# Kernel optimization log

Measured on AMD Instinct MI355X. Metric: run time of the kernel, lower is better.

The kernel has to match this reference:

```python
import jax, jax.numpy as jnp
import numpy as np

E, K = 8, 2            # num_experts, top-k
I, H, O = 1024, 4096, 1024  # input_dim, hidden_dim, output_dim
N = 8192               # batch (tokens)


def _ln(x, g, b, eps=1e-5):
    # torch nn.LayerNorm: biased variance
    m = x.mean(-1, keepdims=True)
    v = x.var(-1, keepdims=True)
    return (x - m) * jax.lax.rsqrt(v + eps) * g + b


def setup_inputs() -> dict:
    key = jax.random.key(0)
    ks = jax.random.split(key, 8)
    s = lambda i, shape, scale: jax.random.normal(ks[i], shape, jnp.float32) * scale
    return dict(
        x=s(0, (N, I), 1.0),
        w1=s(1, (E, I, H), I ** -0.5),
        b1=jnp.zeros((E, H), jnp.float32),
        ln1_g=jnp.ones((E, H), jnp.float32),
        ln1_b=jnp.zeros((E, H), jnp.float32),
        w2=s(2, (E, H, O), H ** -0.5),
        b2=jnp.zeros((E, O), jnp.float32),
        wg=s(3, (I, E), I ** -0.5),
        bg=jnp.zeros((E,), jnp.float32),
        out_g=jnp.ones((O,), jnp.float32),
        out_b=jnp.zeros((O,), jnp.float32),
    )


def reference(x, w1, b1, ln1_g, ln1_b, w2, b2, wg, bg, out_g, out_b):
    n = x.shape[0]
    # gating: softmax -> top-k -> renormalize
    probs = jax.nn.softmax(x @ wg + bg, axis=-1)          # [N, E]
    topw, topi = jax.lax.top_k(probs, K)                  # [N, K]
    topw = topw / topw.sum(-1, keepdims=True)
    rows = jnp.arange(n)[:, None]
    combine = jnp.zeros((n, E), x.dtype).at[rows, topi].add(topw)  # [N, E]
    mask = jnp.zeros((n, E), x.dtype).at[rows, topi].set(1.0)      # [N, E]

    # expert dispatch + weighted combine; combine==0 for unrouted tokens,
    # mathematically identical to the torch gather/index_add loop (eval mode, dropout off)
    def step(acc, p):
        W1, B1, G, Bt, W2, B2, c = p
        h = jax.nn.gelu(_ln(x @ W1 + B1, G, Bt), approximate=False)  # [N, H]
        return acc + c[:, None] * (h @ W2 + B2), None

    out0 = jnp.zeros((n, w2.shape[-1]), x.dtype)
    out, _ = jax.lax.scan(step, out0, (w1, b1, ln1_g, ln1_b, w2, b2, combine.T))

    # aux load-balancing loss (torch .std() is unbiased, ddof=1)
    imp = probs.sum(0)
    imp_loss = (jnp.std(imp, ddof=1) / (imp.mean() + 1e-6)) ** 2
    load = mask.mean(0)
    load_loss = (jnp.std(load, ddof=1) / (load.mean() + 1e-6)) ** 2
    aux = imp_loss + load_loss

    out = _ln(out, out_g, out_b)
    return out, aux
```

## Files before the change

### kernel.cpp

```cpp
#include <hip/hip_runtime.h>

#define NTOK 8192
#define IDIM 1024
#define HDIM 4096
#define ODIM 1024
#define NEXP 8
#define ROWCAP 18432
#define MBLK 72
#define GATE_BLOCKS 512

typedef unsigned short u16;
typedef __attribute__((ext_vector_type(8))) __bf16 bf16x8;
typedef __attribute__((ext_vector_type(8))) short short8;
typedef __attribute__((ext_vector_type(4))) float f32x4;
typedef __attribute__((ext_vector_type(4))) unsigned short u16x4;
typedef __attribute__((ext_vector_type(8))) unsigned short u16x8;

__device__ __forceinline__ u16 f2bf(float f) {
  union { float f; unsigned u; } c; c.f = f;
  unsigned u = c.u;
  return (u16)((u + 0x7fffu + ((u >> 16) & 1u)) >> 16);
}
__device__ __forceinline__ float bf2f(u16 h) {
  union { unsigned u; float f; } c; c.u = ((unsigned)h) << 16;
  return c.f;
}
__device__ __forceinline__ void gload16(const void* g, void* l) {
  __builtin_amdgcn_global_load_lds((const __attribute__((address_space(1))) unsigned*)g,
                                   (__attribute__((address_space(3))) unsigned*)l, 16, 0, 0);
}

#define BARR __builtin_amdgcn_s_barrier()
#define LGKM0 asm volatile("s_waitcnt lgkmcnt(0)" ::: "memory")
#define VMW4 asm volatile("s_waitcnt vmcnt(4)" ::: "memory")
#define VMW0 asm volatile("s_waitcnt vmcnt(0)" ::: "memory")
#define CFENCE asm volatile("" ::: "memory")

#define QUAD(AF, BF, MB, NBQ)                                                   \
  _Pragma("unroll") for (int kk = 0; kk < 2; ++kk)                              \
  _Pragma("unroll") for (int f = 0; f < 4; ++f)                                 \
  _Pragma("unroll") for (int n = 0; n < 2; ++n)                                 \
    acc[(MB) + f][(NBQ) + n] = __builtin_amdgcn_mfma_f32_16x16x32_bf16(         \
        AF[f][kk], BF[n][kk], acc[(MB) + f][(NBQ) + n], 0, 0, 0);

__global__ __launch_bounds__(256) void transpose_convert_kernel(
    const float* __restrict__ w1, const float* __restrict__ w2,
    u16* __restrict__ w1t, u16* __restrict__ w2t) {
  __shared__ __align__(16) unsigned char ldsb[32768];
  int bid = blockIdx.x;
  const float* in; u16* outp; int R, C, r0, c0;
  if (bid < 2048) {
    int e = bid >> 8, t = bid & 255;
    in = w1 + (size_t)e * IDIM * HDIM; outp = w1t + (size_t)e * IDIM * HDIM;
    R = IDIM; C = HDIM;
    r0 = (t >> 5) * 128; c0 = (t & 31) * 128;
  } else {
    int b2 = bid - 2048;
    int e = b2 >> 8, t = b2 & 255;
    in = w2 + (size_t)e * HDIM * ODIM; outp = w2t + (size_t)e * HDIM * ODIM;
    R = HDIM; C = ODIM;
    r0 = (t >> 3) * 128; c0 = (t & 7) * 128;
  }
  int tid = threadIdx.x;
  int rr = tid >> 5, cc = (tid & 31) * 4;
  #pragma unroll
  for (int it = 0; it < 16; ++it) {
    int r = it * 8 + rr;
    f32x4 v = *(const f32x4*)(in + (size_t)(r0 + r) * C + c0 + cc);
    u16x4 o;
    #pragma unroll
    for (int j = 0; j < 4; ++j) o[j] = f2bf(v[j]);
    unsigned a = ((unsigned)(r * 256 + cc * 2)) ^ ((((unsigned)r >> 3) & 7u) << 4);
    *(u16x4*)(ldsb + a) = o;
  }
  __syncthreads();
  int rc = tid & 15, cg = tid >> 4;
  #pragma unroll
  for (int i = 0; i < 8; ++i) {
    int c = cg + i * 16;
    u16x8 o;
    #pragma unroll
    for (int k = 0; k < 8; ++k) {
      int r = rc * 8 + k;
      unsigned a = ((unsigned)(r * 256 + c * 2)) ^ ((((unsigned)r >> 3) & 7u) << 4);
      o[k] = *(const u16*)(ldsb + a);
    }
    *(u16x8*)(outp + (size_t)(c0 + c) * R + r0 + rc * 8) = o;
  }
}

__global__ __launch_bounds__(256) void gating_kernel(
    const float* __restrict__ x, const float* __restrict__ wg, const float* __restrict__ bg,
    float* __restrict__ combine, float* __restrict__ imp_partial,
    int* __restrict__ sel, u16* __restrict__ xb) {
  __shared__ float wgs2[NEXP * IDIM];
  __shared__ float impw[4][NEXP];
  int tid = threadIdx.x;
  for (int d = tid; d < IDIM * NEXP; d += 256) {
    int i4 = d & 255, j = (d >> 8) & 3, e = d >> 10;
    wgs2[d] = wg[(i4 * 4 + j) * 8 + e];
  }
  __syncthreads();
  int wave = tid >> 6, lane = tid & 63;
  float impacc[NEXP];
  #pragma unroll
  for (int e = 0; e < NEXP; ++e) impacc[e] = 0.f;

  for (int it = 0; it < 4; ++it) {
    int t = blockIdx.x * 16 + wave * 4 + it;
    const float* xr = x + (size_t)t * IDIM;
    u16* xbw = xb + (size_t)t * IDIM;
    float s[NEXP];
    #pragma unroll
    for (int e = 0; e < NEXP; ++e) s[e] = 0.f;
    #pragma unroll
    for (int ii = 0; ii < 4; ++ii) {
      int base = ii * 256 + lane * 4;
      f32x4 xv = *(const f32x4*)(xr + base);
      u16x4 o;
      #pragma unroll
      for (int j = 0; j < 4; ++j) o[j] = f2bf(xv[j]);
      *(u16x4*)(xbw + base) = o;
      #pragma unroll
      for (int j = 0; j < 4; ++j) {
        int idx = j * 256 + ii * 64 + lane;
        #pragma unroll
        for (int e = 0; e < NEXP; ++e)
          s[e] = fmaf(xv[j], wgs2[e * 1024 + idx], s[e]);
      }
    }
    #pragma unroll
    for (int e = 0; e < NEXP; ++e) {
      #pragma unroll
      for (int off = 32; off; off >>= 1) s[e] += __shfl_xor(s[e], off);
    }
    if (lane == 0) {
      #pragma unroll
      for (int e = 0; e < NEXP; ++e) s[e] += bg[e];
      int i1 = 0; float v1 = s[0];
      #pragma unroll
      for (int e = 1; e < NEXP; ++e) if (s[e] > v1) { v1 = s[e]; i1 = e; }
      int i2 = -1; float v2 = -1e30f;
      #pragma unroll
      for (int e = 0; e < NEXP; ++e) if (e != i1 && s[e] > v2) { v2 = s[e]; i2 = e; }
      float p[NEXP], sum = 0.f;
      #pragma unroll
      for (int e = 0; e < NEXP; ++e) { p[e] = expf(s[e] - v1); sum += p[e]; }
      float inv = 1.f / sum;
      #pragma unroll
      for (int e = 0; e < NEXP; ++e) { p[e] *= inv; impacc[e] += p[e]; }
      float c1 = 1.f / (1.f + expf(v2 - v1));
      float c2 = 1.f - c1;
      #pragma unroll
      for (int e = 0; e < NEXP; ++e) combine[(size_t)t * NEXP + e] = 0.f;
      combine[(size_t)t * NEXP + i1] = c1;
      combine[(size_t)t * NEXP + i2] = c2;
      sel[t] = i1 | (i2 << 4);
    }
  }
  if (lane == 0) {
    #pragma unroll
    for (int e = 0; e < NEXP; ++e) impw[wave][e] = impacc[e];
  }
  __syncthreads();
  if (tid == 0) {
    #pragma unroll
    for (int e = 0; e < NEXP; ++e)
      imp_partial[blockIdx.x * NEXP + e] = impw[0][e] + impw[1][e] + impw[2][e] + impw[3][e];
  }
}

__global__ __launch_bounds__(256) void compact_kernel(
    const int* __restrict__ sel, int* __restrict__ tokenlist,
    int* __restrict__ cnt, int* __restrict__ pos) {
  __shared__ int warpsum[4];
  int e = blockIdx.x;
  int tid = threadIdx.x, lane = tid & 63, wave = tid >> 6;
  int base = 0;
  for (int chunk = 0; chunk < NTOK; chunk += 256) {
    int t = chunk + tid;
    int s = sel[t];
    int i1 = s & 15, i2 = s >> 4;
    bool m2 = (i2 == e);
    bool m = (i1 == e) || m2;
    unsigned long long bal = __ballot(m);
    int rank = __popcll(bal & ((1ull << lane) - 1ull));
    if (lane == 0) warpsum[wave] = __popcll(bal);
    __syncthreads();
    int woff = 0;
    #pragma unroll
    for (int w = 0; w < 4; ++w) if (w < wave) woff += warpsum[w];
    int total = warpsum[0] + warpsum[1] + warpsum[2] + warpsum[3];
    if (m) {
      int slot = base + woff + rank;
      tokenlist[e * NTOK + slot] = t;
      pos[t * 2 + (m2 ? 1 : 0)] = (e << 16) | slot;
    }
    base += total;
    __syncthreads();
  }
  if (tid == 0) cnt[e] = base;
}

__global__ __launch_bounds__(64) void offsets_aux_kernel(
    const int* __restrict__ cnt, const float* __restrict__ imp_partial,
    int* __restrict__ offsets, float* __restrict__ aux_out) {
  __shared__ float imp[NEXP];
  int tid = threadIdx.x;
  if (tid < NEXP) {
    float v = 0.f;
    for (int b = 0; b < GATE_BLOCKS; ++b) v += imp_partial[b * NEXP + tid];
    imp[tid] = v;
  }
  __syncthreads();
  if (tid == 0) {
    int off = 0;
    for (int e = 0; e < NEXP; ++e) { offsets[e] = off; off += (cnt[e] + 255) & ~255; }
    offsets[NEXP] = off;
    double im = 0.0;
    for (int e = 0; e < NEXP; ++e) im += imp[e];
    im /= NEXP;
    double iv = 0.0;
    for (int e = 0; e < NEXP; ++e) { double d = (double)imp[e] - im; iv += d * d; }
    iv /= (NEXP - 1);
    double il = sqrt(iv) / (im + 1e-6); il = il * il;
    double lm = 0.0;
    for (int e = 0; e < NEXP; ++e) lm += cnt[e];
    lm /= (double)NEXP * NTOK;
    double lv = 0.0;
    for (int e = 0; e < NEXP; ++e) { double d = (double)cnt[e] / NTOK - lm; lv += d * d; }
    lv /= (NEXP - 1);
    double ll = sqrt(lv) / (lm + 1e-6); ll = ll * ll;
    aux_out[0] = (float)(il + ll);
  }
}

__global__ __launch_bounds__(512, 2) void gemm1_kernel(
    const u16* __restrict__ xb, const u16* __restrict__ w1t, const float* __restrict__ b1,
    const int* __restrict__ tokenlist, const int* __restrict__ cnt,
    const int* __restrict__ offsets, u16* __restrict__ Hbuf) {
  __shared__ __align__(64) unsigned char sm[139264];
  const int NB = HDIM / 256;
  const int TT = IDIM / 64;
  int nwg = NB * MBLK;
  int flat = blockIdx.y * NB + blockIdx.x;
  int q = nwg >> 3;
  int swzb = (flat & 7) * q + (flat >> 3);
  int mb = swzb / NB, cb = swzb % NB;
  int grb = mb * 256;
  if (grb >= offsets[NEXP]) return;
  int e = 0;
  #pragma unroll
  for (int k = 0; k < NEXP - 1; ++k) if (grb >= offsets[k + 1]) e = k + 1;
  int lr0 = grb - offsets[e];
  int cnt_e = cnt[e];
  int tid = threadIdx.x, lane = tid & 63, wave = tid >> 6;
  int wr = wave >> 2, wc = wave & 3;

  const int* tl = tokenlist + e * NTOK;
  int colel = (((tid & 7) ^ ((tid >> 3) & 7)) << 3);
  const u16* pA[4]; const u16* pB[4];
  #pragma unroll
  for (int h = 0; h < 2; ++h)
    #pragma unroll
    for (int j = 0; j < 2; ++j) {
      int rowT = h * 128 + j * 64 + (tid >> 3);
      int tok = tl[min(lr0 + rowT, cnt_e - 1)];
      pA[h * 2 + j] = xb + (size_t)tok * IDIM + colel;
      pB[h * 2 + j] = w1t + ((size_t)e * HDIM + cb * 256 + rowT) * IDIM + colel;
    }
  unsigned ldsw = wave * 1024;

  #define STAGE_A(T, H) { unsigned d = (((T) & 1) << 16) + (H) * 16384 + ldsw; \
      gload16(pA[(H)*2+0] + (T)*64, sm + d); gload16(pA[(H)*2+1] + (T)*64, sm + d + 8192); }
  #define STAGE_B(T, H) { unsigned d = (((T) & 1) << 16) + 32768 + (H) * 16384 + ldsw; \
      gload16(pB[(H)*2+0] + (T)*64, sm + d); gload16(pB[(H)*2+1] + (T)*64, sm + d + 8192); }

  int rA = lane & 15;
  int swz = (((lane >> 4) ^ (lane & 7)) << 4);
  int aOff = wr * 16384 + rA * 128 + swz;
  int bOff = 32768 + wc * 8192 + rA * 128 + swz;

  f32x4 acc[8][4];
  #pragma unroll
  for (int m = 0; m < 8; ++m)
    #pragma unroll
    for (int n = 0; n < 4; ++n) acc[m][n] = (f32x4){0.f, 0.f, 0.f, 0.f};
  bf16x8 af[4][2], bf0[2][2], bf1[2][2];

  STAGE_A(0, 0); STAGE_A(0, 1); STAGE_B(0, 0); STAGE_B(0, 1);
  CFENCE;
  STAGE_B(1, 0); STAGE_B(1, 1);
  VMW4; BARR;

  for (int t = 0; t < TT; ++t) {
    int bufb = (t & 1) << 16;
    #pragma unroll
    for (int f = 0; f < 4; ++f) {
      int o = bufb + aOff + f * 2048;
      af[f][0] = *(const bf16x8*)(sm + o);
      af[f][1] = *(const bf16x8*)(sm + (o ^ 64));
    }
    #pragma unroll
    for (int n = 0; n < 2; ++n) {
      int o = bufb + bOff + n * 2048;
      bf0[n][0] = *(const bf16x8*)(sm + o);
      bf0[n][1] = *(const bf16x8*)(sm + (o ^ 64));
    }
    if (t + 1 < TT) STAGE_A(t + 1, 0);
    BARR; LGKM0;
    __builtin_amdgcn_s_setprio(1);
    QUAD(af, bf0, 0, 0);
    __builtin_amdgcn_s_setprio(0);
    #pragma unroll
    for (int n = 0; n < 2; ++n) {
      int o = bufb + bOff + 4096 + n * 2048;
      bf1[n][0] = *(const bf16x8*)(sm + o);
      bf1[n][1] = *(const bf16x8*)(sm + (o ^ 64));
    }
    if (t + 1 < TT) STAGE_A(t + 1, 1);
    BARR; LGKM0;
    __builtin_amdgcn_s_setprio(1);
    QUAD(af, bf1, 0, 2);
    __builtin_amdgcn_s_setprio(0);
    #pragma unroll
    for (int f = 0; f < 4; ++f) {
      int o = bufb + aOff + 8192 + f * 2048;
      af[f][0] = *(const bf16x8*)(sm + o);
      af[f][1] = *(const bf16x8*)(sm + (o ^ 64));
    }
    BARR; LGKM0;
    __builtin_amdgcn_s_setprio(1);
    QUAD(af, bf1, 4, 2);
    __builtin_amdgcn_s_setprio(0);
    if (t + 2 < TT) { STAGE_B(t + 2, 0); STAGE_B(t + 2, 1); }
    __builtin_amdgcn_s_setprio(1);
    QUAD(af, bf0, 4, 0);
    __builtin_amdgcn_s_setprio(0);
    if (t + 2 < TT) { VMW4; } else { VMW0; }
    BARR;
  }

  #pragma unroll
  for (int n = 0; n < 4; ++n) {
    int colb = (wc * 64 + n * 16 + (lane & 15)) * 2;
    float bias = b1[e * HDIM + cb * 256 + wc * 64 + n * 16 + (lane & 15)];
    #pragma unroll
    for (int m = 0; m < 8; ++m) {
      int row = wr * 128 + m * 16 + (lane >> 4) * 4;
      #pragma unroll
      for (int j = 0; j < 4; ++j)
        *(u16*)(sm + (row + j) * 544 + colb) = f2bf(acc[m][n][j] + bias);
    }
  }
  BARR;
  #pragma unroll
  for (int p = 0; p < 16; ++p) {
    int cidx = p * 512 + tid;
    int row = cidx >> 5, cch = cidx & 31;
    u16x8 v = *(const u16x8*)(sm + row * 544 + cch * 16);
    *(u16x8*)(Hbuf + (size_t)(grb + row) * HDIM + cb * 256 + cch * 8) = v;
  }
  #undef STAGE_A
  #undef STAGE_B
}

__global__ __launch_bounds__(512, 2) void gemm2_kernel(
    const u16* __restrict__ Hbuf, const u16* __restrict__ w2t, const float* __restrict__ b2,
    const int* __restrict__ tokenlist, const int* __restrict__ cnt,
    const int* __restrict__ offsets, const float* __restrict__ combine,
    u16* __restrict__ Gout) {
  __shared__ __align__(64) unsigned char sm[139264];
  const int NB = ODIM / 256;
  const int TT = (HDIM / 2) / 64;
  int nwg = NB * MBLK;
  int flat = blockIdx.y * NB + blockIdx.x;
  int q = nwg >> 3;
  int swzb = (flat & 7) * q + (flat >> 3);
  int mb = swzb / NB, cb = swzb % NB;
  int ks = blockIdx.z;
  int grb = mb * 256;
  if (grb >= offsets[NEXP]) return;
  int e = 0;
  #pragma unroll
  for (int k = 0; k < NEXP - 1; ++k) if (grb >= offsets[k + 1]) e = k + 1;
  int lr0 = grb - offsets[e];
  int cnt_e = cnt[e];
  int tid = threadIdx.x, lane = tid & 63, wave = tid >> 6;
  int wr = wave >> 2, wc = wave & 3;
  size_t ksOff = (size_t)ks * (HDIM / 2);
  u16* Gk = Gout + (size_t)ks * ROWCAP * ODIM;

  int colel = (((tid & 7) ^ ((tid >> 3) & 7)) << 3);
  const u16* pA[4]; const u16* pB[4];
  #pragma unroll
  for (int h = 0; h < 2; ++h)
    #pragma unroll
    for (int j = 0; j < 2; ++j) {
      int rowT = h * 128 + j * 64 + (tid >> 3);
      pA[h * 2 + j] = Hbuf + (size_t)(grb + rowT) * HDIM + ksOff + colel;
      pB[h * 2 + j] = w2t + ((size_t)e * ODIM + cb * 256 + rowT) * HDIM + ksOff + colel;
    }
  unsigned ldsw = wave * 1024;

  #define STAGE_A(T, H) { unsigned d = (((T) & 1) << 16) + (H) * 16384 + ldsw; \
      gload16(pA[(H)*2+0] + (T)*64, sm + d); gload16(pA[(H)*2+1] + (T)*64, sm + d + 8192); }
  #define STAGE_B(T, H) { unsigned d = (((T) & 1) << 16) + 32768 + (H) * 16384 + ldsw; \
      gload16(pB[(H)*2+0] + (T)*64, sm + d); gload16(pB[(H)*2+1] + (T)*64, sm + d + 8192); }

  int rA = lane & 15;
  int swz = (((lane >> 4) ^ (lane & 7)) << 4);
  int aOff = wr * 16384 + rA * 128 + swz;
  int bOff = 32768 + wc * 8192 + rA * 128 + swz;

  f32x4 acc[8][4];
  #pragma unroll
  for (int m = 0; m < 8; ++m)
    #pragma unroll
    for (int n = 0; n < 4; ++n) acc[m][n] = (f32x4){0.f, 0.f, 0.f, 0.f};
  bf16x8 af[4][2], bf0[2][2], bf1[2][2];

  STAGE_A(0, 0); STAGE_A(0, 1); STAGE_B(0, 0); STAGE_B(0, 1);
  CFENCE;
  STAGE_B(1, 0); STAGE_B(1, 1);
  VMW4; BARR;

  for (int t = 0; t < TT; ++t) {
    int bufb = (t & 1) << 16;
    #pragma unroll
    for (int f = 0; f < 4; ++f) {
      int o = bufb + aOff + f * 2048;
      af[f][0] = *(const bf16x8*)(sm + o);
      af[f][1] = *(const bf16x8*)(sm + (o ^ 64));
    }
    #pragma unroll
    for (int n = 0; n < 2; ++n) {
      int o = bufb + bOff + n * 2048;
      bf0[n][0] = *(const bf16x8*)(sm + o);
      bf0[n][1] = *(const bf16x8*)(sm + (o ^ 64));
    }
    if (t + 1 < TT) STAGE_A(t + 1, 0);
    BARR; LGKM0;
    __builtin_amdgcn_s_setprio(1);
    QUAD(af, bf0, 0, 0);
    __builtin_amdgcn_s_setprio(0);
    #pragma unroll
    for (int n = 0; n < 2; ++n) {
      int o = bufb + bOff + 4096 + n * 2048;
      bf1[n][0] = *(const bf16x8*)(sm + o);
      bf1[n][1] = *(const bf16x8*)(sm + (o ^ 64));
    }
    if (t + 1 < TT) STAGE_A(t + 1, 1);
    BARR; LGKM0;
    __builtin_amdgcn_s_setprio(1);
    QUAD(af, bf1, 0, 2);
    __builtin_amdgcn_s_setprio(0);
    #pragma unroll
    for (int f = 0; f < 4; ++f) {
      int o = bufb + aOff + 8192 + f * 2048;
      af[f][0] = *(const bf16x8*)(sm + o);
      af[f][1] = *(const bf16x8*)(sm + (o ^ 64));
    }
    BARR; LGKM0;
    __builtin_amdgcn_s_setprio(1);
    QUAD(af, bf1, 4, 2);
    __builtin_amdgcn_s_setprio(0);
    if (t + 2 < TT) { STAGE_B(t + 2, 0); STAGE_B(t + 2, 1); }
    __builtin_amdgcn_s_setprio(1);
    QUAD(af, bf0, 4, 0);
    __builtin_amdgcn_s_setprio(0);
    if (t + 2 < TT) { VMW4; } else { VMW0; }
    BARR;
  }

  const int* tl = tokenlist + e * NTOK;
  float bias_n[4];
  #pragma unroll
  for (int n = 0; n < 4; ++n)
    bias_n[n] = (ks == 0) ? b2[e * ODIM + cb * 256 + wc * 64 + n * 16 + (lane & 15)] : 0.f;
  #pragma unroll
  for (int m = 0; m < 8; ++m) {
    #pragma unroll
    for (int j = 0; j < 4; ++j) {
      int rr = wr * 128 + m * 16 + (lane >> 4) * 4 + j;
      int tok = tl[min(lr0 + rr, cnt_e - 1)];
      float c = combine[(size_t)tok * NEXP + e];
      #pragma unroll
      for (int n = 0; n < 4; ++n)
        *(u16*)(sm + rr * 544 + (wc * 64 + n * 16 + (lane & 15)) * 2) =
            f2bf(c * (acc[m][n][j] + bias_n[n]));
    }
  }
  BARR;
  #pragma unroll
  for (int p = 0; p < 16; ++p) {
    int cidx = p * 512 + tid;
    int row = cidx >> 5, cch = cidx & 31;
    u16x8 v = *(const u16x8*)(sm + row * 544 + cch * 16);
    *(u16x8*)(Gk + (size_t)(grb + row) * ODIM + cb * 256 + cch * 8) = v;
  }
  #undef STAGE_A
  #undef STAGE_B
}

__global__ __launch_bounds__(256) void ln_gelu_kernel(
    u16* __restrict__ Hbuf, const float* __restrict__ g, const float* __restrict__ b,
    const int* __restrict__ offsets) {
  int r = blockIdx.x;
  if (r >= offsets[NEXP]) return;
  int e = 0;
  #pragma unroll
  for (int k = 0; k < NEXP - 1; ++k) if (r >= offsets[k + 1]) e = k + 1;
  u16* row = Hbuf + (size_t)r * HDIM;
  const float* ge = g + e * HDIM;
  const float* be = b + e * HDIM;
  int tid = threadIdx.x;
  float s = 0.f, ss = 0.f;
  short8 v[2];
  #pragma unroll
  for (int it = 0; it < 2; ++it) {
    v[it] = *(const short8*)(row + (tid + it * 256) * 8);
    #pragma unroll
    for (int j = 0; j < 8; ++j) { float f = bf2f((u16)v[it][j]); s += f; ss += f * f; }
  }
  #pragma unroll
  for (int off = 32; off; off >>= 1) { s += __shfl_xor(s, off); ss += __shfl_xor(ss, off); }
  __shared__ float rs[4], rss[4];
  int wave = tid >> 6, lane = tid & 63;
  if (lane == 0) { rs[wave] = s; rss[wave] = ss; }
  __syncthreads();
  float S = rs[0] + rs[1] + rs[2] + rs[3];
  float SS = rss[0] + rss[1] + rss[2] + rss[3];
  float mean = S * (1.f / HDIM);
  float var = SS * (1.f / HDIM) - mean * mean;
  float rstd = rsqrtf(var + 1e-5f);
  #pragma unroll
  for (int it = 0; it < 2; ++it) {
    int base = (tid + it * 256) * 8;
    f32x4 g0 = *(const f32x4*)(ge + base);
    f32x4 g1 = *(const f32x4*)(ge + base + 4);
    f32x4 b0 = *(const f32x4*)(be + base);
    f32x4 b1v = *(const f32x4*)(be + base + 4);
    u16x8 o;
    #pragma unroll
    for (int j = 0; j < 8; ++j) {
      float f = bf2f((u16)v[it][j]);
      float gg = j < 4 ? g0[j & 3] : g1[j & 3];
      float bb = j < 4 ? b0[j & 3] : b1v[j & 3];
      float y = (f - mean) * rstd * gg + bb;
      float gel = 0.5f * y * (1.f + erff(y * 0.70710678118654752f));
      o[j] = f2bf(gel);
    }
    *(u16x8*)(row + base) = o;
  }
}

__global__ __launch_bounds__(256) void final_ln_kernel(
    const u16* __restrict__ Gout, const int* __restrict__ pos,
    const int* __restrict__ offsets, const float* __restrict__ g,
    const float* __restrict__ b, float* __restrict__ out) {
  const size_t SPLIT = (size_t)ROWCAP * ODIM;
  int t = blockIdx.x;
  int tid = threadIdx.x;
  int p1 = pos[t * 2 + 0];
  int p2 = pos[t * 2 + 1];
  size_t r1 = (size_t)(offsets[p1 >> 16] + (p1 & 0xFFFF)) * ODIM + tid * 4;
  size_t r2 = (size_t)(offsets[p2 >> 16] + (p2 & 0xFFFF)) * ODIM + tid * 4;
  u16x4 a0 = *(const u16x4*)(Gout + r1);
  u16x4 a1 = *(const u16x4*)(Gout + SPLIT + r1);
  u16x4 c0 = *(const u16x4*)(Gout + r2);
  u16x4 c1 = *(const u16x4*)(Gout + SPLIT + r2);
  f32x4 v;
  #pragma unroll
  for (int j = 0; j < 4; ++j)
    v[j] = bf2f(a0[j]) + bf2f(a1[j]) + bf2f(c0[j]) + bf2f(c1[j]);
  float s = v[0] + v[1] + v[2] + v[3];
  float ss = v[0] * v[0] + v[1] * v[1] + v[2] * v[2] + v[3] * v[3];
  #pragma unroll
  for (int off = 32; off; off >>= 1) { s += __shfl_xor(s, off); ss += __shfl_xor(ss, off); }
  __shared__ float rs[4], rss[4];
  int wave = tid >> 6, lane = tid & 63;
  if (lane == 0) { rs[wave] = s; rss[wave] = ss; }
  __syncthreads();
  float S = rs[0] + rs[1] + rs[2] + rs[3];
  float SS = rss[0] + rss[1] + rss[2] + rss[3];
  float mean = S * (1.f / ODIM);
  float var = SS * (1.f / ODIM) - mean * mean;
  float rstd = rsqrtf(var + 1e-5f);
  f32x4 gv = *(const f32x4*)(g + tid * 4);
  f32x4 bv = *(const f32x4*)(b + tid * 4);
  f32x4 o;
  #pragma unroll
  for (int j = 0; j < 4; ++j) o[j] = (v[j] - mean) * rstd * gv[j] + bv[j];
  *(f32x4*)(out + (size_t)t * ODIM + tid * 4) = o;
}

extern "C" void kernel_launch(void* const* d_in, const int* in_sizes, int n_in,
                              void* d_out, int out_size, void* d_ws, size_t ws_size,
                              hipStream_t stream) {
  (void)in_sizes; (void)n_in; (void)out_size; (void)ws_size;
  const float* x    = (const float*)d_in[0];
  const float* w1   = (const float*)d_in[1];
  const float* b1   = (const float*)d_in[2];
  const float* ln1g = (const float*)d_in[3];
  const float* ln1b = (const float*)d_in[4];
  const float* w2   = (const float*)d_in[5];
  const float* b2   = (const float*)d_in[6];
  const float* wg   = (const float*)d_in[7];
  const float* bg   = (const float*)d_in[8];
  const float* outg = (const float*)d_in[9];
  const float* outb = (const float*)d_in[10];
  float* out = (float*)d_out;

  char* ws = (char*)d_ws;
  size_t off = 0;
  auto alloc = [&](size_t bytes) {
    char* p = ws + off;
    off += (bytes + 255) & ~(size_t)255;
    return p;
  };
  size_t xb_sz  = (size_t)NTOK * IDIM * 2;
  size_t w1t_sz = (size_t)NEXP * HDIM * IDIM * 2;
  size_t gout_sz = (size_t)2 * ROWCAP * ODIM * 2;
  size_t reg0 = xb_sz + w1t_sz;
  if (gout_sz > reg0) reg0 = gout_sz;
  char* base0 = (char*)alloc(reg0);
  u16* xb   = (u16*)base0;
  u16* w1t  = (u16*)(base0 + xb_sz);
  u16* Gout = (u16*)base0;

  u16* w2t       = (u16*)alloc((size_t)NEXP * ODIM * HDIM * 2);
  u16* Hbuf      = (u16*)alloc((size_t)ROWCAP * HDIM * 2);
  float* combine = (float*)alloc((size_t)NTOK * NEXP * 4);
  int* tokenlist = (int*)alloc((size_t)NEXP * NTOK * 4);
  int* pos       = (int*)alloc((size_t)NTOK * 2 * 4);
  int* sel       = (int*)alloc((size_t)NTOK * 4);
  int* cnt       = (int*)alloc(64);
  int* offsets   = (int*)alloc(64);
  float* imp_partial = (float*)alloc(GATE_BLOCKS * NEXP * 4);

  hipMemsetAsync(cnt, 0, 64, stream);

  transpose_convert_kernel<<<4096, 256, 0, stream>>>(w1, w2, w1t, w2t);
  gating_kernel<<<GATE_BLOCKS, 256, 0, stream>>>(x, wg, bg, combine, imp_partial, sel, xb);
  compact_kernel<<<NEXP, 256, 0, stream>>>(sel, tokenlist, cnt, pos);
  offsets_aux_kernel<<<1, 64, 0, stream>>>(cnt, imp_partial, offsets, out + (size_t)NTOK * ODIM);
  gemm1_kernel<<<dim3(HDIM / 256, MBLK), 512, 0, stream>>>(xb, w1t, b1, tokenlist, cnt, offsets, Hbuf);
  ln_gelu_kernel<<<ROWCAP, 256, 0, stream>>>(Hbuf, ln1g, ln1b, offsets);
  gemm2_kernel<<<dim3(ODIM / 256, MBLK, 2), 512, 0, stream>>>(Hbuf, w2t, b2, tokenlist, cnt, offsets, combine, Gout);
  final_ln_kernel<<<NTOK, 256, 0, stream>>>(Gout, pos, offsets, outg, outb, out);
}
```

Before: 530.7 us.

## Enlarge per-wave gemm2 tile to 128x128 with 4 waves and vectorize gating

```diff
diff --git a/kernel.cpp b/kernel.cpp
--- a/kernel.cpp
+++ b/kernel.cpp
@@ -33,6 +33,7 @@
 #define BARR __builtin_amdgcn_s_barrier()
 #define LGKM0 asm volatile("s_waitcnt lgkmcnt(0)" ::: "memory")
 #define VMW4 asm volatile("s_waitcnt vmcnt(4)" ::: "memory")
+#define VMW8 asm volatile("s_waitcnt vmcnt(8)" ::: "memory")
 #define VMW0 asm volatile("s_waitcnt vmcnt(0)" ::: "memory")
 #define CFENCE asm volatile("" ::: "memory")
 
@@ -93,19 +94,18 @@
     const float* __restrict__ x, const float* __restrict__ wg, const float* __restrict__ bg,
     float* __restrict__ combine, float* __restrict__ imp_partial,
     int* __restrict__ sel, u16* __restrict__ xb) {
-  __shared__ float wgs2[NEXP * IDIM];
+  __shared__ float wgs3[NEXP * IDIM];
   __shared__ float impw[4][NEXP];
   int tid = threadIdx.x;
-  for (int d = tid; d < IDIM * NEXP; d += 256) {
-    int i4 = d & 255, j = (d >> 8) & 3, e = d >> 10;
-    wgs2[d] = wg[(i4 * 4 + j) * 8 + e];
-  }
+  for (int d = tid; d < IDIM * NEXP; d += 256)
+    wgs3[d] = wg[(d & 1023) * 8 + (d >> 10)];
   __syncthreads();
   int wave = tid >> 6, lane = tid & 63;
   float impacc[NEXP];
   #pragma unroll
   for (int e = 0; e < NEXP; ++e) impacc[e] = 0.f;
 
+  #pragma unroll
   for (int it = 0; it < 4; ++it) {
     int t = blockIdx.x * 16 + wave * 4 + it;
     const float* xr = x + (size_t)t * IDIM;
@@ -121,12 +121,14 @@
       #pragma unroll
       for (int j = 0; j < 4; ++j) o[j] = f2bf(xv[j]);
       *(u16x4*)(xbw + base) = o;
-      #pragma unroll
-      for (int j = 0; j < 4; ++j) {
-        int idx = j * 256 + ii * 64 + lane;
-        #pragma unroll
-        for (int e = 0; e < NEXP; ++e)
-          s[e] = fmaf(xv[j], wgs2[e * 1024 + idx], s[e]);
+      const float* wp = wgs3 + (size_t)(ii * 64 + lane) * 4;
+      #pragma unroll
+      for (int e = 0; e < NEXP; ++e) {
+        f32x4 wv = *(const f32x4*)(wp + e * 1024);
+        s[e] = fmaf(xv[0], wv[0], s[e]);
+        s[e] = fmaf(xv[1], wv[1], s[e]);
+        s[e] = fmaf(xv[2], wv[2], s[e]);
+        s[e] = fmaf(xv[3], wv[3], s[e]);
       }
     }
     #pragma unroll
@@ -365,7 +367,7 @@
   #undef STAGE_B
 }
 
-__global__ __launch_bounds__(512, 2) void gemm2_kernel(
+__global__ __launch_bounds__(256, 1) void gemm2_kernel(
     const u16* __restrict__ Hbuf, const u16* __restrict__ w2t, const float* __restrict__ b2,
     const int* __restrict__ tokenlist, const int* __restrict__ cnt,
     const int* __restrict__ offsets, const float* __restrict__ combine,
@@ -387,43 +389,41 @@
   int lr0 = grb - offsets[e];
   int cnt_e = cnt[e];
   int tid = threadIdx.x, lane = tid & 63, wave = tid >> 6;
-  int wr = wave >> 2, wc = wave & 3;
+  int wr = wave >> 1, wc = wave & 1;
   size_t ksOff = (size_t)ks * (HDIM / 2);
   u16* Gk = Gout + (size_t)ks * ROWCAP * ODIM;
 
   int colel = (((tid & 7) ^ ((tid >> 3) & 7)) << 3);
-  const u16* pA[4]; const u16* pB[4];
-  #pragma unroll
-  for (int h = 0; h < 2; ++h)
-    #pragma unroll
-    for (int j = 0; j < 2; ++j) {
-      int rowT = h * 128 + j * 64 + (tid >> 3);
-      pA[h * 2 + j] = Hbuf + (size_t)(grb + rowT) * HDIM + ksOff + colel;
-      pB[h * 2 + j] = w2t + ((size_t)e * ODIM + cb * 256 + rowT) * HDIM + ksOff + colel;
-    }
-  unsigned ldsw = wave * 1024;
-
-  #define STAGE_A(T, H) { unsigned d = (((T) & 1) << 16) + (H) * 16384 + ldsw; \
-      gload16(pA[(H)*2+0] + (T)*64, sm + d); gload16(pA[(H)*2+1] + (T)*64, sm + d + 8192); }
-  #define STAGE_B(T, H) { unsigned d = (((T) & 1) << 16) + 32768 + (H) * 16384 + ldsw; \
-      gload16(pB[(H)*2+0] + (T)*64, sm + d); gload16(pB[(H)*2+1] + (T)*64, sm + d + 8192); }
+  const u16* pAb = Hbuf + (size_t)(grb + (tid >> 3)) * HDIM + ksOff + colel;
+  const u16* pBb = w2t + ((size_t)e * ODIM + cb * 256 + (tid >> 3)) * HDIM + ksOff + colel;
+
+  #define STAGE_A(T, H) { unsigned d = (((T) & 1) << 16) + (H) * 16384 + wave * 1024;      \
+      gload16(pAb + (size_t)((H) * 128 + 0)  * HDIM + (T) * 64, sm + d + 0);               \
+      gload16(pAb + (size_t)((H) * 128 + 32) * HDIM + (T) * 64, sm + d + 4096);            \
+      gload16(pAb + (size_t)((H) * 128 + 64) * HDIM + (T) * 64, sm + d + 8192);            \
+      gload16(pAb + (size_t)((H) * 128 + 96) * HDIM + (T) * 64, sm + d + 12288); }
+  #define STAGE_B(T, H) { unsigned d = (((T) & 1) << 16) + 32768 + (H) * 16384 + wave * 1024; \
+      gload16(pBb + (size_t)((H) * 128 + 0)  * HDIM + (T) * 64, sm + d + 0);               \
+      gload16(pBb + (size_t)((H) * 128 + 32) * HDIM + (T) * 64, sm + d + 4096);            \
+      gload16(pBb + (size_t)((H) * 128 + 64) * HDIM + (T) * 64, sm + d + 8192);            \
+      gload16(pBb + (size_t)((H) * 128 + 96) * HDIM + (T) * 64, sm + d + 12288); }
 
   int rA = lane & 15;
   int swz = (((lane >> 4) ^ (lane & 7)) << 4);
   int aOff = wr * 16384 + rA * 128 + swz;
-  int bOff = 32768 + wc * 8192 + rA * 128 + swz;
-
-  f32x4 acc[8][4];
+  int bOff = 32768 + wc * 16384 + rA * 128 + swz;
+
+  f32x4 acc[8][8];
   #pragma unroll
   for (int m = 0; m < 8; ++m)
     #pragma unroll
-    for (int n = 0; n < 4; ++n) acc[m][n] = (f32x4){0.f, 0.f, 0.f, 0.f};
-  bf16x8 af[4][2], bf0[2][2], bf1[2][2];
+    for (int n = 0; n < 8; ++n) acc[m][n] = (f32x4){0.f, 0.f, 0.f, 0.f};
+  bf16x8 af[8][2], bf[4][2];
 
   STAGE_A(0, 0); STAGE_A(0, 1); STAGE_B(0, 0); STAGE_B(0, 1);
   CFENCE;
   STAGE_B(1, 0); STAGE_B(1, 1);
-  VMW4; BARR;
+  VMW8; BARR;
 
   for (int t = 0; t < TT; ++t) {
     int bufb = (t & 1) << 16;
@@ -434,50 +434,54 @@
       af[f][1] = *(const bf16x8*)(sm + (o ^ 64));
     }
     #pragma unroll
-    for (int n = 0; n < 2; ++n) {
+    for (int n = 0; n < 4; ++n) {
       int o = bufb + bOff + n * 2048;
-      bf0[n][0] = *(const bf16x8*)(sm + o);
-      bf0[n][1] = *(const bf16x8*)(sm + (o ^ 64));
+      bf[n][0] = *(const bf16x8*)(sm + o);
+      bf[n][1] = *(const bf16x8*)(sm + (o ^ 64));
     }
     if (t + 1 < TT) STAGE_A(t + 1, 0);
     BARR; LGKM0;
     __builtin_amdgcn_s_setprio(1);
-    QUAD(af, bf0, 0, 0);
-    __builtin_amdgcn_s_setprio(0);
-    #pragma unroll
-    for (int n = 0; n < 2; ++n) {
-      int o = bufb + bOff + 4096 + n * 2048;
-      bf1[n][0] = *(const bf16x8*)(sm + o);
-      bf1[n][1] = *(const bf16x8*)(sm + (o ^ 64));
+    QUAD(af, bf, 0, 0);
+    QUAD(af, (bf + 2), 0, 2);
+    __builtin_amdgcn_s_setprio(0);
+    #pragma unroll
+    for (int f = 0; f < 4; ++f) {
+      int o = bufb + aOff + 8192 + f * 2048;
+      af[4 + f][0] = *(const bf16x8*)(sm + o);
+      af[4 + f][1] = *(const bf16x8*)(sm + (o ^ 64));
     }
     if (t + 1 < TT) STAGE_A(t + 1, 1);
     BARR; LGKM0;
     __builtin_amdgcn_s_setprio(1);
-    QUAD(af, bf1, 0, 2);
-    __builtin_amdgcn_s_setprio(0);
-    #pragma unroll
-    for (int f = 0; f < 4; ++f) {
-      int o = bufb + aOff + 8192 + f * 2048;
-      af[f][0] = *(const bf16x8*)(sm + o);
-      af[f][1] = *(const bf16x8*)(sm + (o ^ 64));
+    QUAD((af + 4), bf, 4, 0);
+    QUAD((af + 4), (bf + 2), 4, 2);
+    __builtin_amdgcn_s_setprio(0);
+    #pragma unroll
+    for (int n = 0; n < 4; ++n) {
+      int o = bufb + bOff + 8192 + n * 2048;
+      bf[n][0] = *(const bf16x8*)(sm + o);
+      bf[n][1] = *(const bf16x8*)(sm + (o ^ 64));
     }
     BARR; LGKM0;
     __builtin_amdgcn_s_setprio(1);
-    QUAD(af, bf1, 4, 2);
+    QUAD((af + 4), bf, 4, 4);
+    QUAD((af + 4), (bf + 2), 4, 6);
     __builtin_amdgcn_s_setprio(0);
     if (t + 2 < TT) { STAGE_B(t + 2, 0); STAGE_B(t + 2, 1); }
     __builtin_amdgcn_s_setprio(1);
-    QUAD(af, bf0, 4, 0);
-    __builtin_amdgcn_s_setprio(0);
-    if (t + 2 < TT) { VMW4; } else { VMW0; }
+    QUAD(af, bf, 0, 4);
+    QUAD(af, (bf + 2), 0, 6);
+    __builtin_amdgcn_s_setprio(0);
+    if (t + 2 < TT) { VMW8; } else { VMW0; }
     BARR;
   }
 
   const int* tl = tokenlist + e * NTOK;
-  float bias_n[4];
-  #pragma unroll
-  for (int n = 0; n < 4; ++n)
-    bias_n[n] = (ks == 0) ? b2[e * ODIM + cb * 256 + wc * 64 + n * 16 + (lane & 15)] : 0.f;
+  float bias_n[8];
+  #pragma unroll
+  for (int n = 0; n < 8; ++n)
+    bias_n[n] = (ks == 0) ? b2[e * ODIM + cb * 256 + wc * 128 + n * 16 + (lane & 15)] : 0.f;
   #pragma unroll
   for (int m = 0; m < 8; ++m) {
     #pragma unroll
@@ -486,15 +490,15 @@
       int tok = tl[min(lr0 + rr, cnt_e - 1)];
       float c = combine[(size_t)tok * NEXP + e];
       #pragma unroll
-      for (int n = 0; n < 4; ++n)
-        *(u16*)(sm + rr * 544 + (wc * 64 + n * 16 + (lane & 15)) * 2) =
+      for (int n = 0; n < 8; ++n)
+        *(u16*)(sm + rr * 544 + (wc * 128 + n * 16 + (lane & 15)) * 2) =
             f2bf(c * (acc[m][n][j] + bias_n[n]));
     }
   }
   BARR;
   #pragma unroll
-  for (int p = 0; p < 16; ++p) {
-    int cidx = p * 512 + tid;
+  for (int p = 0; p < 32; ++p) {
+    int cidx = p * 256 + tid;
     int row = cidx >> 5, cch = cidx & 31;
     u16x8 v = *(const u16x8*)(sm + row * 544 + cch * 16);
     *(u16x8*)(Gk + (size_t)(grb + row) * ODIM + cb * 256 + cch * 8) = v;
@@ -639,14 +643,12 @@
   int* offsets   = (int*)alloc(64);
   float* imp_partial = (float*)alloc(GATE_BLOCKS * NEXP * 4);
 
-  hipMemsetAsync(cnt, 0, 64, stream);
-
   transpose_convert_kernel<<<4096, 256, 0, stream>>>(w1, w2, w1t, w2t);
   gating_kernel<<<GATE_BLOCKS, 256, 0, stream>>>(x, wg, bg, combine, imp_partial, sel, xb);
   compact_kernel<<<NEXP, 256, 0, stream>>>(sel, tokenlist, cnt, pos);
   offsets_aux_kernel<<<1, 64, 0, stream>>>(cnt, imp_partial, offsets, out + (size_t)NTOK * ODIM);
   gemm1_kernel<<<dim3(HDIM / 256, MBLK), 512, 0, stream>>>(xb, w1t, b1, tokenlist, cnt, offsets, Hbuf);
   ln_gelu_kernel<<<ROWCAP, 256, 0, stream>>>(Hbuf, ln1g, ln1b, offsets);
-  gemm2_kernel<<<dim3(ODIM / 256, MBLK, 2), 512, 0, stream>>>(Hbuf, w2t, b2, tokenlist, cnt, offsets, combine, Gout);
+  gemm2_kernel<<<dim3(ODIM / 256, MBLK, 2), 256, 0, stream>>>(Hbuf, w2t, b2, tokenlist, cnt, offsets, combine, Gout);
   final_ln_kernel<<<NTOK, 256, 0, stream>>>(Gout, pos, offsets, outg, outb, out);
 }
```

Result: slower. 567.1 us (+6.8%).
